# Kernel optimization log

Hardware: AMD Instinct MI355X
Metric: run time of the kernel (lower is better)

The kernel has to match this reference:

```python
import jax, jax.numpy as jnp
import numpy as np
from jax import lax

T, B, C, L = 2048, 96, 128, 128
BLANK = 0
SMOOTHING = 0.1
NEG = jnp.float32(-1e30)  # finite stand-in for -inf (safe grads, bf16-safe exponent)


def setup_inputs() -> dict:
    key = jax.random.key(0)
    k1, k2 = jax.random.split(key)
    logits = jax.random.normal(k1, (T, B, C), dtype=jnp.float32)
    log_probs = jax.nn.log_softmax(logits, axis=-1)  # [T,B,C], properly normalized
    targets = jax.random.randint(k2, (B, L), 1, C, dtype=jnp.int32)  # labels, never blank
    input_lengths = jnp.full((B,), T, dtype=jnp.int32)
    target_lengths = jnp.full((B,), L, dtype=jnp.int32)
    return {"log_probs": log_probs, "targets": targets,
            "input_lengths": input_lengths, "target_lengths": target_lengths}


def _ctc_loss(log_probs, targets, input_lengths, target_lengths):
    """Per-sample CTC negative log-likelihood. targets: [B, L] dense."""
    S = 2 * L + 1  # extended label length: blank-interleaved
    # extended labels [B, S]: blank, y1, blank, y2, ..., yL, blank
    ext = jnp.full((B, S), BLANK, dtype=jnp.int32).at[:, 1::2].set(targets)
    # gather log-probs of extended labels: [T, B, S]
    lp_ext = jnp.take_along_axis(log_probs, jnp.broadcast_to(ext[None], (T, B, S)), axis=2)
    # skip (s-2 -> s) transition allowed iff label(s) != blank and label(s) != label(s-2)
    same2 = jnp.concatenate([jnp.ones((B, 2), bool), ext[:, 2:] == ext[:, :-2]], axis=1)
    can_skip = (ext != BLANK) & (~same2)  # [B, S]

    alpha0 = jnp.full((B, S), NEG, dtype=log_probs.dtype)
    alpha0 = alpha0.at[:, 0].set(lp_ext[0, :, 0]).at[:, 1].set(lp_ext[0, :, 1])

    negcol1 = jnp.full((B, 1), NEG, dtype=log_probs.dtype)
    negcol2 = jnp.full((B, 2), NEG, dtype=log_probs.dtype)

    def step(alpha, xs):
        lp_t, t = xs  # lp_t: [B, S]
        a1 = jnp.concatenate([negcol1, alpha[:, :-1]], axis=1)
        a2 = jnp.where(can_skip, jnp.concatenate([negcol2, alpha[:, :-2]], axis=1), NEG)
        new = jnp.logaddexp(jnp.logaddexp(alpha, a1), a2) + lp_t
        active = (t < input_lengths)[:, None]  # freeze past each sample's length
        return jnp.where(active, new, alpha), None

    alphaT, _ = lax.scan(step, alpha0, (lp_ext[1:], jnp.arange(1, T)))
    bidx = jnp.arange(B)
    ll = jnp.logaddexp(alphaT[bidx, 2 * target_lengths],
                       alphaT[bidx, 2 * target_lengths - 1])  # [B]
    # zero_infinity: impossible alignments -> loss 0
    return jnp.where(ll < NEG / 2, 0.0, -ll)


def reference(log_probs, targets, input_lengths, target_lengths):
    ctc = _ctc_loss(log_probs, targets, input_lengths, target_lengths)  # [B]
    # label-smoothing KL(uniform-over-nonblank || p) pointwise term,
    # torch: kl_div(input=log_probs, target=u).sum(-1) = sum_c u*(log u - log p_c), u_blank = 0
    u = 1.0 / (C - 1)
    nonblank = (jnp.arange(C) != BLANK)  # [C]
    kl = jnp.sum(jnp.where(nonblank, u * (jnp.log(jnp.float32(u)) - log_probs), 0.0), axis=-1)  # [T,B]
    tmask = (jnp.arange(T)[:, None] < input_lengths[None, :]).astype(kl.dtype)  # [T,B]
    kl_mean = jnp.sum(kl * tmask, axis=0) / input_lengths.astype(kl.dtype)  # [B]
    loss = (1.0 - SMOOTHING) * ctc + SMOOTHING * kl_mean
    return loss.mean()
```

## Files before the change

### kernel.cpp

```cpp
#include <hip/hip_runtime.h>
#include <math.h>

#define T_DIM 2048
#define B_DIM 96
#define C_DIM 128
#define L_DIM 128
#define LOG2E 1.4426950408889634f
#define LN2 0.69314718055994531f
#define SMOOTH 0.1f
#define SENT (-(1 << 30))
#define NPH 32

#define AOFF 0
#define BOFF 24672
#define KLA  49344
#define KLB  49440
#define LOSS 49536

__device__ __forceinline__ float dpp_shr1_f(float x) {
  return __int_as_float(__builtin_amdgcn_update_dpp(
      0, __float_as_int(x), 0x138 , 0xF, 0xF, true));
}
__device__ __forceinline__ float dpp_shl1_f(float x) {
  return __int_as_float(__builtin_amdgcn_update_dpp(
      0, __float_as_int(x), 0x130 , 0xF, 0xF, true));
}

#define ALPHA_STEP(kk_) do {                                                 \
  const int k_ = (kk_);                                                      \
  const float pAv = fA[k_ & 3], pBv = fB[k_ & 3], pKv = fK[k_ & 3];          \
  {                                                                          \
    const int kn = k_ + 4;                                                   \
    const float* nr = (kn < 32) ? (pc + kn * C_DIM)                          \
                                : (pn + (kn - 32) * C_DIM);                  \
    fA[k_ & 3] = nr[tgA]; fB[k_ & 3] = nr[tgB]; fK[k_ & 3] = nr[0];          \
  }                                                                          \
  const float r3s = dpp_shr1_f(r3);                                          \
  const int   Es  = (int)dpp_shr1_f((float)E);                               \
  const int   be  = (__float_as_int(r3s) >> 23) & 0xFF;                      \
  int diff = (be - 187) + (Es - E);                                          \
  diff = (__float_as_int(r3s) != 0 && diff > 0) ? diff : 0;                  \
  r0 = ldexpf(r0, -diff); r1 = ldexpf(r1, -diff); r2 = ldexpf(r2, -diff);    \
  r3 = ldexpf(r3, -diff); r4 = ldexpf(r4, -diff);                            \
  E += diff;                                                                 \
  const float d3 = ldexpf(r3s, Es - E);                                      \
  const float n0 = (r0 + d3) * pKv;                                          \
  const float n1 = __builtin_fmaf(skA, d3, r0 + r1) * pAv;                   \
  const float n2 = (r2 + r1) * pKv;                                          \
  const float n3 = __builtin_fmaf(skB, r1, r3 + r2) * pBv;                   \
  const float n4 = (r4 + r3) * pKv;                                          \
  r0 = n0; r1 = n1; r2 = n2; r3 = n3; r4 = n4;                               \
  if ((k_ & 3) == 3) {                                                       \
    const float m = fmaxf(fmaxf(fmaxf(r0, r1), fmaxf(r2, r3)), r4);          \
    const int sh2 = (m > 0.0f)                                               \
                      ? (187 - ((__float_as_int(m) >> 23) & 0xFF)) : 0;      \
    r0 = ldexpf(r0, sh2); r1 = ldexpf(r1, sh2); r2 = ldexpf(r2, sh2);        \
    r3 = ldexpf(r3, sh2); r4 = ldexpf(r4, sh2);                              \
    E -= sh2;                                                                \
  }                                                                          \
} while (0)

#define BETA_STEP(kk_) do {                                                  \
  const int k_ = (kk_);                                                      \
  const float pAv = fA[k_ & 3], pBv = fB[k_ & 3], pKv = fK[k_ & 3];          \
  const float pNv = fN[k_ & 3];                                              \
  {                                                                          \
    const int kn = k_ + 4;                                                   \
    const float* nr = (kn < 32) ? (pc + kn * C_DIM)                          \
                                : (pn + (kn - 32) * C_DIM);                  \
    fA[k_ & 3] = nr[tgA]; fB[k_ & 3] = nr[tgB]; fK[k_ & 3] = nr[0];          \
    fN[k_ & 3] = nr[tgAn];                                                   \
  }                                                                          \
  const float r1s = dpp_shl1_f(r1);                                          \
  const int   Es  = (int)dpp_shl1_f((float)E);                               \
  const int   be  = (__float_as_int(r1s) >> 23) & 0xFF;                      \
  int diff = (be - 187) + (Es - E);                                          \
  diff = (__float_as_int(r1s) != 0 && diff > 0) ? diff : 0;                  \
  r0 = ldexpf(r0, -diff); r1 = ldexpf(r1, -diff); r2 = ldexpf(r2, -diff);    \
  r3 = ldexpf(r3, -diff); r4 = ldexpf(r4, -diff);                            \
  E += diff;                                                                 \
  const float d5 = ldexpf(r1s, Es - E);                                      \
  const float g0 = r0 * pKv, g1 = r1 * pAv, g2 = r2 * pKv;                   \
  const float g3 = r3 * pBv, g4 = r4 * pKv, g5 = d5 * pNv;                   \
  const float n0 = g0 + g1;                                                  \
  const float n1 = __builtin_fmaf(skAp, g3, g1 + g2);                        \
  const float n2 = g2 + g3;                                                  \
  const float n3 = __builtin_fmaf(skBp, g5, g3 + g4);                        \
  const float n4 = g4 + g5;                                                  \
  r0 = n0; r1 = n1; r2 = n2; r3 = n3; r4 = n4;                               \
  if ((k_ & 3) == 3) {                                                       \
    const float m = fmaxf(fmaxf(fmaxf(r0, r1), fmaxf(r2, r3)), r4);          \
    const int sh2 = (m > 0.0f)                                               \
                      ? (187 - ((__float_as_int(m) >> 23) & 0xFF)) : 0;      \
    r0 = ldexpf(r0, sh2); r1 = ldexpf(r1, sh2); r2 = ldexpf(r2, sh2);        \
    r3 = ldexpf(r3, sh2); r4 = ldexpf(r4, sh2);                              \
    E -= sh2;                                                                \
  }                                                                          \
} while (0)

__global__ __launch_bounds__(256) void ctc_fused_kernel(
    const float* __restrict__ lp, const int* __restrict__ targets,
    const int* __restrict__ in_len, const int* __restrict__ tg_len,
    float* __restrict__ ws)
{
  const int tid = threadIdx.x;
  const int bid = blockIdx.x;
  const int isBeta = (bid >= B_DIM);
  const int b = isBeta ? bid - B_DIM : bid;
  const size_t RSTR = (size_t)B_DIM * C_DIM;
  const int Tb = in_len[b];
  const float* base = lp + (size_t)b * C_DIM;

  __shared__ float rows[3][32][C_DIM];
  __shared__ float klred[3];

  float klacc = 0.f;

  if (!isBeta) {
    const int TbA = (Tb < 1024) ? Tb : 1024;
    int tgA = 0, tgB = 0;
    float skA = 0.f, skB = 0.f;
    float r0 = 0.f, r1 = 0.f, r2 = 0.f, r3 = 0.f, r4 = 0.f;
    int E = SENT;
    float fA[4], fB[4], fK[4];

    if (tid < 64) {
      const int l = tid;
      tgA = targets[b * L_DIM + 2 * l];
      tgB = targets[b * L_DIM + 2 * l + 1];
      skA = (l > 0 && tgA != targets[b * L_DIM + 2 * l - 1]) ? 1.f : 0.f;
      skB = (tgB != tgA) ? 1.f : 0.f;
      if (l == 0) {
        r0 = __builtin_amdgcn_exp2f(base[0]   * LOG2E);
        r1 = __builtin_amdgcn_exp2f(base[tgA] * LOG2E);
        E = 0;
      }
    } else {
      const int ptid = tid - 64;
      #pragma unroll
      for (int i = 0; i < 11; ++i) {
        const int task = i * 192 + ptid;
        if (task < 2048) {
          const int row = task >> 5;
          const int c4  = task & 31;
          const int t   = 1 + row;
          const float4 v = *(const float4*)(base + (size_t)t * RSTR + c4 * 4);
          float4 w;
          w.x = __builtin_amdgcn_exp2f(v.x * LOG2E);
          w.y = __builtin_amdgcn_exp2f(v.y * LOG2E);
          w.z = __builtin_amdgcn_exp2f(v.z * LOG2E);
          w.w = __builtin_amdgcn_exp2f(v.w * LOG2E);
          *(float4*)&rows[row >> 5][row & 31][c4 * 4] = w;
          if (t < Tb) {
            float s = v.x + v.y + v.z + v.w;
            if (c4 == 0) s -= v.x;
            klacc += s;
          }
        }
      }
      if (ptid < 32 && 0 < Tb) {
        const float4 v = *(const float4*)(base + ptid * 4);
        float s = v.x + v.y + v.z + v.w;
        if (ptid == 0) s -= v.x;
        klacc += s;
      }
    }
    __syncthreads();

    if (tid < 64) {
      #pragma unroll
      for (int j = 0; j < 4; ++j) {
        fA[j] = rows[0][j][tgA]; fB[j] = rows[0][j][tgB]; fK[j] = rows[0][j][0];
      }
    }
    float* pc = &rows[0][0][0];
    float* pn = &rows[1][0][0];
    float* pf = &rows[2][0][0];

    for (int p = 0; p < NPH; ++p) {
      if (tid < 64) {
        if (32 * p + 33 <= TbA) {
          #pragma unroll
          for (int k = 0; k < 32; ++k) { ALPHA_STEP(k); }
        } else {
          #pragma unroll
          for (int k = 0; k < 32; ++k) {
            const int t = 1 + 32 * p + k;
            if (t < TbA) { ALPHA_STEP(k); }
          }
        }
      } else {
        const int ptid = tid - 64;
        const int t0 = 65 + 32 * p;
        if (t0 <= 1023) {
          #pragma unroll
          for (int i = 0; i < 6; ++i) {
            const int task = i * 192 + ptid;
            if (task < 1024) {
              const int row = task >> 5;
              const int c4  = task & 31;
              const int t   = t0 + row;
              if (t <= 1023) {
                const float4 v = *(const float4*)(base + (size_t)t * RSTR + c4 * 4);
                float4 w;
                w.x = __builtin_amdgcn_exp2f(v.x * LOG2E);
                w.y = __builtin_amdgcn_exp2f(v.y * LOG2E);
                w.z = __builtin_amdgcn_exp2f(v.z * LOG2E);
                w.w = __builtin_amdgcn_exp2f(v.w * LOG2E);
                *(float4*)&pf[row * C_DIM + c4 * 4] = w;
                if (t < Tb) {
                  float s = v.x + v.y + v.z + v.w;
                  if (c4 == 0) s -= v.x;
                  klacc += s;
                }
              }
            }
          }
        }
      }
      __syncthreads();
      float* tmp = pc; pc = pn; pn = pf; pf = tmp;
    }

    if (tid < 64) {
      const int l = tid;
      const float Ef = (float)E;
      float* dst = ws + AOFF + b * 257;
      dst[4 * l + 0] = __builtin_amdgcn_logf(r0) + Ef;
      dst[4 * l + 1] = __builtin_amdgcn_logf(r1) + Ef;
      dst[4 * l + 2] = __builtin_amdgcn_logf(r2) + Ef;
      dst[4 * l + 3] = __builtin_amdgcn_logf(r3) + Ef;
      if (l == 63) dst[256] = __builtin_amdgcn_logf(r4) + Ef;
    } else {
      float tot = klacc;
      tot += __shfl_xor(tot, 1, 64);  tot += __shfl_xor(tot, 2, 64);
      tot += __shfl_xor(tot, 4, 64);  tot += __shfl_xor(tot, 8, 64);
      tot += __shfl_xor(tot, 16, 64); tot += __shfl_xor(tot, 32, 64);
      if ((tid & 63) == 0) klred[(tid >> 6) - 1] = tot;
    }
    __syncthreads();
    if (tid == 0) ws[KLA + b] = klred[0] + klred[1] + klred[2];

  } else {
    int tgA = 0, tgB = 0, tgAn = 0;
    float skAp = 0.f, skBp = 0.f;
    float r0 = 0.f, r1 = 0.f, r2 = 0.f, r3 = 0.f, r4 = 0.f;
    int E = SENT;
    float fA[4], fB[4], fK[4], fN[4];

    if (tid < 64) {
      const int l = tid;
      tgA = targets[b * L_DIM + 2 * l];
      tgB = targets[b * L_DIM + 2 * l + 1];
      const int nidx = (l < 63) ? (2 * l + 2) : (2 * l);
      tgAn = targets[b * L_DIM + nidx];
      skAp = (tgB != tgA) ? 1.f : 0.f;
      skBp = (l < 63 && tgAn != tgB) ? 1.f : 0.f;
      const int Lt = tg_len[b];
      const int s0 = 4 * l;
      r0 = (s0 == 2 * Lt || s0 == 2 * Lt - 1) ? 1.f : 0.f;
      r1 = (s0 + 1 == 2 * Lt || s0 + 1 == 2 * Lt - 1) ? 1.f : 0.f;
      r2 = (s0 + 2 == 2 * Lt || s0 + 2 == 2 * Lt - 1) ? 1.f : 0.f;
      r3 = (s0 + 3 == 2 * Lt || s0 + 3 == 2 * Lt - 1) ? 1.f : 0.f;
      r4 = (s0 + 4 == 2 * Lt || s0 + 4 == 2 * Lt - 1) ? 1.f : 0.f;
      E = (r0 + r1 + r2 + r3 + r4 > 0.f) ? 0 : SENT;
    } else {
      const int ptid = tid - 64;
      #pragma unroll
      for (int i = 0; i < 11; ++i) {
        const int task = i * 192 + ptid;
        if (task < 2048) {
          const int row = task >> 5;
          const int c4  = task & 31;
          const int t   = 2047 - row;
          const float4 v = *(const float4*)(base + (size_t)t * RSTR + c4 * 4);
          float4 w;
          w.x = __builtin_amdgcn_exp2f(v.x * LOG2E);
          w.y = __builtin_amdgcn_exp2f(v.y * LOG2E);
          w.z = __builtin_amdgcn_exp2f(v.z * LOG2E);
          w.w = __builtin_amdgcn_exp2f(v.w * LOG2E);
          *(float4*)&rows[row >> 5][row & 31][c4 * 4] = w;
          if (t < Tb) {
            float s = v.x + v.y + v.z + v.w;
            if (c4 == 0) s -= v.x;
            klacc += s;
          }
        }
      }
    }
    __syncthreads();

    if (tid < 64) {
      #pragma unroll
      for (int j = 0; j < 4; ++j) {
        fA[j] = rows[0][j][tgA]; fB[j] = rows[0][j][tgB];
        fK[j] = rows[0][j][0];   fN[j] = rows[0][j][tgAn];
      }
    }
    float* pc = &rows[0][0][0];
    float* pn = &rows[1][0][0];
    float* pf = &rows[2][0][0];

    for (int p = 0; p < NPH; ++p) {
      if (tid < 64) {
        const int rmax = 2047 - 32 * p;
        const int rmin = rmax - 31;
        if (rmax < Tb) {
          #pragma unroll
          for (int k = 0; k < 32; ++k) { BETA_STEP(k); }
        } else if (rmin < Tb) {
          #pragma unroll
          for (int k = 0; k < 32; ++k) {
            const int r = 2047 - 32 * p - k;
            if (r < Tb) { BETA_STEP(k); }
          }
        }
      } else {
        const int ptid = tid - 64;
        const int t0 = 1983 - 32 * p;
        if (t0 >= 1024) {
          #pragma unroll
          for (int i = 0; i < 6; ++i) {
            const int task = i * 192 + ptid;
            if (task < 1024) {
              const int row = task >> 5;
              const int c4  = task & 31;
              const int t   = t0 - row;
              if (t >= 1024) {
                const float4 v = *(const float4*)(base + (size_t)t * RSTR + c4 * 4);
                float4 w;
                w.x = __builtin_amdgcn_exp2f(v.x * LOG2E);
                w.y = __builtin_amdgcn_exp2f(v.y * LOG2E);
                w.z = __builtin_amdgcn_exp2f(v.z * LOG2E);
                w.w = __builtin_amdgcn_exp2f(v.w * LOG2E);
                *(float4*)&pf[row * C_DIM + c4 * 4] = w;
                if (t < Tb) {
                  float s = v.x + v.y + v.z + v.w;
                  if (c4 == 0) s -= v.x;
                  klacc += s;
                }
              }
            }
          }
        }
      }
      __syncthreads();
      float* tmp = pc; pc = pn; pn = pf; pf = tmp;
    }

    if (tid < 64) {
      const int l = tid;
      const float Ef = (float)E;
      float* dst = ws + BOFF + b * 257;
      dst[4 * l + 0] = __builtin_amdgcn_logf(r0) + Ef;
      dst[4 * l + 1] = __builtin_amdgcn_logf(r1) + Ef;
      dst[4 * l + 2] = __builtin_amdgcn_logf(r2) + Ef;
      dst[4 * l + 3] = __builtin_amdgcn_logf(r3) + Ef;
      if (l == 63) dst[256] = __builtin_amdgcn_logf(r4) + Ef;
    } else {
      float tot = klacc;
      tot += __shfl_xor(tot, 1, 64);  tot += __shfl_xor(tot, 2, 64);
      tot += __shfl_xor(tot, 4, 64);  tot += __shfl_xor(tot, 8, 64);
      tot += __shfl_xor(tot, 16, 64); tot += __shfl_xor(tot, 32, 64);
      if ((tid & 63) == 0) klred[(tid >> 6) - 1] = tot;
    }
    __syncthreads();
    if (tid == 0) ws[KLB + b] = klred[0] + klred[1] + klred[2];
  }
}

__global__ __launch_bounds__(64) void ctc_combine_kernel(
    const float* __restrict__ ws_in, const int* __restrict__ in_len,
    float* __restrict__ ws_out)
{
  const int b = blockIdx.x;
  const int l = threadIdx.x;
  const float* a  = ws_in + AOFF + b * 257;
  const float* bb = ws_in + BOFF + b * 257;
  float x0 = a[4 * l + 0] + bb[4 * l + 0];
  float x1 = a[4 * l + 1] + bb[4 * l + 1];
  float x2 = a[4 * l + 2] + bb[4 * l + 2];
  float x3 = a[4 * l + 3] + bb[4 * l + 3];
  float x4 = (l == 63) ? (a[256] + bb[256]) : -3.0e38f;
  float m = fmaxf(fmaxf(fmaxf(x0, x1), fmaxf(x2, x3)), x4);
  m = fmaxf(m, __shfl_xor(m, 1, 64));  m = fmaxf(m, __shfl_xor(m, 2, 64));
  m = fmaxf(m, __shfl_xor(m, 4, 64));  m = fmaxf(m, __shfl_xor(m, 8, 64));
  m = fmaxf(m, __shfl_xor(m, 16, 64)); m = fmaxf(m, __shfl_xor(m, 32, 64));
  const float ms = fmaxf(m, -1.0e37f);
  float s = __builtin_amdgcn_exp2f(x0 - ms) + __builtin_amdgcn_exp2f(x1 - ms)
          + __builtin_amdgcn_exp2f(x2 - ms) + __builtin_amdgcn_exp2f(x3 - ms)
          + __builtin_amdgcn_exp2f(x4 - ms);
  s += __shfl_xor(s, 1, 64);  s += __shfl_xor(s, 2, 64);
  s += __shfl_xor(s, 4, 64);  s += __shfl_xor(s, 8, 64);
  s += __shfl_xor(s, 16, 64); s += __shfl_xor(s, 32, 64);
  if (l == 0) {
    float ctc = 0.f;
    if (s > 0.f && m > -1.0e30f) {
      ctc = -((ms + __builtin_amdgcn_logf(s)) * LN2);
    }
    const int Tb = in_len[b];
    const float u    = 1.0f / (C_DIM - 1);
    const float logu = -4.8441870864585910f;
    const float kls  = ws_in[KLA + b] + ws_in[KLB + b];
    const float klmean = logu - u * kls / (float)Tb;
    ws_out[LOSS + b] = (1.0f - SMOOTH) * ctc + SMOOTH * klmean;
  }
}

__global__ __launch_bounds__(128) void ctc_mean_kernel(
    const float* __restrict__ ws, float* __restrict__ out)
{
  __shared__ float red[128];
  const int tid = threadIdx.x;
  red[tid] = (tid < B_DIM) ? ws[LOSS + tid] : 0.f;
  __syncthreads();
  for (int off = 64; off > 0; off >>= 1) {
    if (tid < off) red[tid] += red[tid + off];
    __syncthreads();
  }
  if (tid == 0) out[0] = red[0] / (float)B_DIM;
}

extern "C" void kernel_launch(void* const* d_in, const int* in_sizes, int n_in,
                              void* d_out, int out_size, void* d_ws, size_t ws_size,
                              hipStream_t stream) {
  const float* lp      = (const float*)d_in[0];
  const int* targets   = (const int*)d_in[1];
  const int* in_len    = (const int*)d_in[2];
  const int* tg_len    = (const int*)d_in[3];
  float* ws  = (float*)d_ws;
  float* out = (float*)d_out;

  hipLaunchKernelGGL(ctc_fused_kernel, dim3(2 * B_DIM), dim3(256), 0, stream,
                     lp, targets, in_len, tg_len, ws);
  hipLaunchKernelGGL(ctc_combine_kernel, dim3(B_DIM), dim3(64), 0, stream,
                     ws, in_len, ws);
  hipLaunchKernelGGL(ctc_mean_kernel, dim3(1), dim3(128), 0, stream,
                     ws, out);
}
```

Baseline: 88.68 us.

## Merge alpha and beta blocks into one 512-thread block per sample

Instead of launching separate 256-thread blocks for the forward (alpha) and backward (beta) halves, each sample now gets one 512-thread block. The two 256-thread groups run the alpha and beta recursions with separate dynamic shared-memory ring buffers. This halves the block count to 96, so on a GPU with many CUs fewer CUs are used, but both halves share a block. Each __syncthreads now couples the two independent halves, which can add stall time, and the larger 96KB shared footprint limits residency.

```diff
diff --git a/kernel.cpp b/kernel.cpp
--- a/kernel.cpp
+++ b/kernel.cpp
@@ -98,25 +98,26 @@
   }                                                                          \
 } while (0)
 
-__global__ __launch_bounds__(256) void ctc_fused_kernel(
+__global__ __launch_bounds__(512, 2) void ctc_fused_kernel(
     const float* __restrict__ lp, const int* __restrict__ targets,
     const int* __restrict__ in_len, const int* __restrict__ tg_len,
     float* __restrict__ ws)
 {
-  const int tid = threadIdx.x;
-  const int bid = blockIdx.x;
-  const int isBeta = (bid >= B_DIM);
-  const int b = isBeta ? bid - B_DIM : bid;
+  extern __shared__ float dyn[];
+  const int tid  = threadIdx.x;
+  const int grp  = tid >> 8;
+  const int gtid = tid & 255;
+  const int b = blockIdx.x;
   const size_t RSTR = (size_t)B_DIM * C_DIM;
   const int Tb = in_len[b];
   const float* base = lp + (size_t)b * C_DIM;
 
-  __shared__ float rows[3][32][C_DIM];
-  __shared__ float klred[3];
+  float* ring = dyn + grp * (3 * 32 * C_DIM);
+  __shared__ float klred[2][3];
 
   float klacc = 0.f;
 
-  if (!isBeta) {
+  if (grp == 0) {
     const int TbA = (Tb < 1024) ? Tb : 1024;
     int tgA = 0, tgB = 0;
     float skA = 0.f, skB = 0.f;
@@ -124,8 +125,8 @@
     int E = SENT;
     float fA[4], fB[4], fK[4];
 
-    if (tid < 64) {
-      const int l = tid;
+    if (gtid < 64) {
+      const int l = gtid;
       tgA = targets[b * L_DIM + 2 * l];
       tgB = targets[b * L_DIM + 2 * l + 1];
       skA = (l > 0 && tgA != targets[b * L_DIM + 2 * l - 1]) ? 1.f : 0.f;
@@ -136,7 +137,7 @@
         E = 0;
       }
     } else {
-      const int ptid = tid - 64;
+      const int ptid = gtid - 64;
       #pragma unroll
       for (int i = 0; i < 11; ++i) {
         const int task = i * 192 + ptid;
@@ -150,7 +151,7 @@
           w.y = __builtin_amdgcn_exp2f(v.y * LOG2E);
           w.z = __builtin_amdgcn_exp2f(v.z * LOG2E);
           w.w = __builtin_amdgcn_exp2f(v.w * LOG2E);
-          *(float4*)&rows[row >> 5][row & 31][c4 * 4] = w;
+          *(float4*)&ring[(row >> 5) * 32 * C_DIM + (row & 31) * C_DIM + c4 * 4] = w;
           if (t < Tb) {
             float s = v.x + v.y + v.z + v.w;
             if (c4 == 0) s -= v.x;
@@ -167,18 +168,19 @@
     }
     __syncthreads();
 
-    if (tid < 64) {
+    if (gtid < 64) {
       #pragma unroll
       for (int j = 0; j < 4; ++j) {
-        fA[j] = rows[0][j][tgA]; fB[j] = rows[0][j][tgB]; fK[j] = rows[0][j][0];
-      }
-    }
-    float* pc = &rows[0][0][0];
-    float* pn = &rows[1][0][0];
-    float* pf = &rows[2][0][0];
+        fA[j] = ring[j * C_DIM + tgA]; fB[j] = ring[j * C_DIM + tgB];
+        fK[j] = ring[j * C_DIM];
+      }
+    }
+    float* pc = ring;
+    float* pn = ring + 32 * C_DIM;
+    float* pf = ring + 64 * C_DIM;
 
     for (int p = 0; p < NPH; ++p) {
-      if (tid < 64) {
+      if (gtid < 64) {
         if (32 * p + 33 <= TbA) {
           #pragma unroll
           for (int k = 0; k < 32; ++k) { ALPHA_STEP(k); }
@@ -190,7 +192,7 @@
           }
         }
       } else {
-        const int ptid = tid - 64;
+        const int ptid = gtid - 64;
         const int t0 = 65 + 32 * p;
         if (t0 <= 1023) {
           #pragma unroll
@@ -222,8 +224,8 @@
       float* tmp = pc; pc = pn; pn = pf; pf = tmp;
     }
 
-    if (tid < 64) {
-      const int l = tid;
+    if (gtid < 64) {
+      const int l = gtid;
       const float Ef = (float)E;
       float* dst = ws + AOFF + b * 257;
       dst[4 * l + 0] = __builtin_amdgcn_logf(r0) + Ef;
@@ -236,10 +238,10 @@
       tot += __shfl_xor(tot, 1, 64);  tot += __shfl_xor(tot, 2, 64);
       tot += __shfl_xor(tot, 4, 64);  tot += __shfl_xor(tot, 8, 64);
       tot += __shfl_xor(tot, 16, 64); tot += __shfl_xor(tot, 32, 64);
-      if ((tid & 63) == 0) klred[(tid >> 6) - 1] = tot;
+      if ((gtid & 63) == 0) klred[0][(gtid >> 6) - 1] = tot;
     }
     __syncthreads();
-    if (tid == 0) ws[KLA + b] = klred[0] + klred[1] + klred[2];
+    if (gtid == 0) ws[KLA + b] = klred[0][0] + klred[0][1] + klred[0][2];
 
   } else {
     int tgA = 0, tgB = 0, tgAn = 0;
@@ -248,8 +250,8 @@
     int E = SENT;
     float fA[4], fB[4], fK[4], fN[4];
 
-    if (tid < 64) {
-      const int l = tid;
+    if (gtid < 64) {
+      const int l = gtid;
       tgA = targets[b * L_DIM + 2 * l];
       tgB = targets[b * L_DIM + 2 * l + 1];
       const int nidx = (l < 63) ? (2 * l + 2) : (2 * l);
@@ -265,7 +267,7 @@
       r4 = (s0 + 4 == 2 * Lt || s0 + 4 == 2 * Lt - 1) ? 1.f : 0.f;
       E = (r0 + r1 + r2 + r3 + r4 > 0.f) ? 0 : SENT;
     } else {
-      const int ptid = tid - 64;
+      const int ptid = gtid - 64;
       #pragma unroll
       for (int i = 0; i < 11; ++i) {
         const int task = i * 192 + ptid;
@@ -279,7 +281,7 @@
           w.y = __builtin_amdgcn_exp2f(v.y * LOG2E);
           w.z = __builtin_amdgcn_exp2f(v.z * LOG2E);
           w.w = __builtin_amdgcn_exp2f(v.w * LOG2E);
-          *(float4*)&rows[row >> 5][row & 31][c4 * 4] = w;
+          *(float4*)&ring[(row >> 5) * 32 * C_DIM + (row & 31) * C_DIM + c4 * 4] = w;
           if (t < Tb) {
             float s = v.x + v.y + v.z + v.w;
             if (c4 == 0) s -= v.x;
@@ -290,19 +292,19 @@
     }
     __syncthreads();
 
-    if (tid < 64) {
+    if (gtid < 64) {
       #pragma unroll
       for (int j = 0; j < 4; ++j) {
-        fA[j] = rows[0][j][tgA]; fB[j] = rows[0][j][tgB];
-        fK[j] = rows[0][j][0];   fN[j] = rows[0][j][tgAn];
-      }
-    }
-    float* pc = &rows[0][0][0];
-    float* pn = &rows[1][0][0];
-    float* pf = &rows[2][0][0];
+        fA[j] = ring[j * C_DIM + tgA]; fB[j] = ring[j * C_DIM + tgB];
+        fK[j] = ring[j * C_DIM];       fN[j] = ring[j * C_DIM + tgAn];
+      }
+    }
+    float* pc = ring;
+    float* pn = ring + 32 * C_DIM;
+    float* pf = ring + 64 * C_DIM;
 
     for (int p = 0; p < NPH; ++p) {
-      if (tid < 64) {
+      if (gtid < 64) {
         const int rmax = 2047 - 32 * p;
         const int rmin = rmax - 31;
         if (rmax < Tb) {
@@ -316,7 +318,7 @@
           }
         }
       } else {
-        const int ptid = tid - 64;
+        const int ptid = gtid - 64;
         const int t0 = 1983 - 32 * p;
         if (t0 >= 1024) {
           #pragma unroll
@@ -348,8 +350,8 @@
       float* tmp = pc; pc = pn; pn = pf; pf = tmp;
     }
 
-    if (tid < 64) {
-      const int l = tid;
+    if (gtid < 64) {
+      const int l = gtid;
       const float Ef = (float)E;
       float* dst = ws + BOFF + b * 257;
       dst[4 * l + 0] = __builtin_amdgcn_logf(r0) + Ef;
@@ -362,10 +364,10 @@
       tot += __shfl_xor(tot, 1, 64);  tot += __shfl_xor(tot, 2, 64);
       tot += __shfl_xor(tot, 4, 64);  tot += __shfl_xor(tot, 8, 64);
       tot += __shfl_xor(tot, 16, 64); tot += __shfl_xor(tot, 32, 64);
-      if ((tid & 63) == 0) klred[(tid >> 6) - 1] = tot;
+      if ((gtid & 63) == 0) klred[1][(gtid >> 6) - 1] = tot;
     }
     __syncthreads();
-    if (tid == 0) ws[KLB + b] = klred[0] + klred[1] + klred[2];
+    if (gtid == 0) ws[KLB + b] = klred[1][0] + klred[1][1] + klred[1][2];
   }
 }
 
@@ -431,7 +433,16 @@
   float* ws  = (float*)d_ws;
   float* out = (float*)d_out;
 
-  hipLaunchKernelGGL(ctc_fused_kernel, dim3(2 * B_DIM), dim3(256), 0, stream,
+  const size_t dynBytes = 2u * 3u * 32u * C_DIM * sizeof(float);
+  static bool attrSet = false;
+  if (!attrSet) {
+    (void)hipFuncSetAttribute((const void*)ctc_fused_kernel,
+                              hipFuncAttributeMaxDynamicSharedMemorySize,
+                              (int)dynBytes);
+    attrSet = true;
+  }
+
+  hipLaunchKernelGGL(ctc_fused_kernel, dim3(B_DIM), dim3(512), dynBytes, stream,
                      lp, targets, in_len, tg_len, ws);
   hipLaunchKernelGGL(ctc_combine_kernel, dim3(B_DIM), dim3(64), 0, stream,
                      ws, in_len, ws);
```

New measurement: 139.9 us. 57.7% more time.

## Amortize per-step exponent alignment into a once-per-4-steps neighbor scale exchange

Applied to the files above, without the earlier changes.

Each alpha and beta step used to exchange the neighbor lane's exponent over DPP and rescale all five registers with ldexp before using the shifted value. Now the exponent alignment runs only every four steps, alongside the existing renormalization, and yields a multiplicative scale factor. The per-step neighbor term becomes a single multiply. This shortens the serial dependency chain of the recurrence, at the cost of a lower renormalization target exponent and more reliance on float headroom between syncs.

```diff
diff --git a/kernel.cpp b/kernel.cpp
--- a/kernel.cpp
+++ b/kernel.cpp
@@ -9,6 +9,7 @@
 #define LN2 0.69314718055994531f
 #define SMOOTH 0.1f
 #define SENT (-(1 << 30))
+#define SENTF (-1073741824.0f)
 #define NPH 32
 
 #define AOFF 0
@@ -25,6 +26,50 @@
   return __int_as_float(__builtin_amdgcn_update_dpp(
       0, __float_as_int(x), 0x130 , 0xF, 0xF, true));
 }
+
+#define AEXCH() do {                                                         \
+  const float m = fmaxf(fmaxf(fmaxf(r0, r1), fmaxf(r2, r3)), r4);            \
+  const int sh2 = (m > 0.0f) ? (177 - ((__float_as_int(m) >> 23) & 0xFF)) : 0;\
+  r0 = ldexpf(r0, sh2); r1 = ldexpf(r1, sh2); r2 = ldexpf(r2, sh2);          \
+  r3 = ldexpf(r3, sh2); r4 = ldexpf(r4, sh2);                                \
+  E -= sh2;                                                                  \
+  float Esf = dpp_shr1_f((float)E);                                          \
+  Esf = (tid == 0) ? SENTF : Esf;                                            \
+  const int Es = (int)Esf;                                                   \
+  const bool live = (Es != SENT);                                            \
+  if (E == SENT && live) E = Es;                                             \
+  int sh = (Es - E) - 60; sh = (sh > 0) ? sh : 0; sh = (sh > 252) ? 252 : sh;\
+  r0 = ldexpf(r0, -sh); r1 = ldexpf(r1, -sh); r2 = ldexpf(r2, -sh);          \
+  r3 = ldexpf(r3, -sh); r4 = ldexpf(r4, -sh);                                \
+  E += sh;                                                                   \
+  const int diff = Es - E;                                                   \
+  int dc = (diff < -126) ? -126 : diff;                                      \
+  float sc = __int_as_float((127 + dc) << 23);                               \
+  sc = (diff < -126) ? 0.0f : sc;                                            \
+  scale = live ? sc : 0.0f;                                                  \
+} while (0)
+
+#define BEXCH() do {                                                         \
+  const float m = fmaxf(fmaxf(fmaxf(r0, r1), fmaxf(r2, r3)), r4);            \
+  const int sh2 = (m > 0.0f) ? (177 - ((__float_as_int(m) >> 23) & 0xFF)) : 0;\
+  r0 = ldexpf(r0, sh2); r1 = ldexpf(r1, sh2); r2 = ldexpf(r2, sh2);          \
+  r3 = ldexpf(r3, sh2); r4 = ldexpf(r4, sh2);                                \
+  E -= sh2;                                                                  \
+  float Esf = dpp_shl1_f((float)E);                                          \
+  Esf = (tid == 63) ? SENTF : Esf;                                           \
+  const int Es = (int)Esf;                                                   \
+  const bool live = (Es != SENT);                                            \
+  if (E == SENT && live) E = Es;                                             \
+  int sh = (Es - E) - 60; sh = (sh > 0) ? sh : 0; sh = (sh > 252) ? 252 : sh;\
+  r0 = ldexpf(r0, -sh); r1 = ldexpf(r1, -sh); r2 = ldexpf(r2, -sh);          \
+  r3 = ldexpf(r3, -sh); r4 = ldexpf(r4, -sh);                                \
+  E += sh;                                                                   \
+  const int diff = Es - E;                                                   \
+  int dc = (diff < -126) ? -126 : diff;                                      \
+  float sc = __int_as_float((127 + dc) << 23);                               \
+  sc = (diff < -126) ? 0.0f : sc;                                            \
+  scale = live ? sc : 0.0f;                                                  \
+} while (0)
 
 #define ALPHA_STEP(kk_) do {                                                 \
   const int k_ = (kk_);                                                      \
@@ -36,28 +81,14 @@
     fA[k_ & 3] = nr[tgA]; fB[k_ & 3] = nr[tgB]; fK[k_ & 3] = nr[0];          \
   }                                                                          \
   const float r3s = dpp_shr1_f(r3);                                          \
-  const int   Es  = (int)dpp_shr1_f((float)E);                               \
-  const int   be  = (__float_as_int(r3s) >> 23) & 0xFF;                      \
-  int diff = (be - 187) + (Es - E);                                          \
-  diff = (__float_as_int(r3s) != 0 && diff > 0) ? diff : 0;                  \
-  r0 = ldexpf(r0, -diff); r1 = ldexpf(r1, -diff); r2 = ldexpf(r2, -diff);    \
-  r3 = ldexpf(r3, -diff); r4 = ldexpf(r4, -diff);                            \
-  E += diff;                                                                 \
-  const float d3 = ldexpf(r3s, Es - E);                                      \
+  const float d3  = r3s * scale;                                             \
   const float n0 = (r0 + d3) * pKv;                                          \
   const float n1 = __builtin_fmaf(skA, d3, r0 + r1) * pAv;                   \
   const float n2 = (r2 + r1) * pKv;                                          \
   const float n3 = __builtin_fmaf(skB, r1, r3 + r2) * pBv;                   \
   const float n4 = (r4 + r3) * pKv;                                          \
   r0 = n0; r1 = n1; r2 = n2; r3 = n3; r4 = n4;                               \
-  if ((k_ & 3) == 3) {                                                       \
-    const float m = fmaxf(fmaxf(fmaxf(r0, r1), fmaxf(r2, r3)), r4);          \
-    const int sh2 = (m > 0.0f)                                               \
-                      ? (187 - ((__float_as_int(m) >> 23) & 0xFF)) : 0;      \
-    r0 = ldexpf(r0, sh2); r1 = ldexpf(r1, sh2); r2 = ldexpf(r2, sh2);        \
-    r3 = ldexpf(r3, sh2); r4 = ldexpf(r4, sh2);                              \
-    E -= sh2;                                                                \
-  }                                                                          \
+  if ((k_ & 3) == 3) { AEXCH(); }                                            \
 } while (0)
 
 #define BETA_STEP(kk_) do {                                                  \
@@ -72,14 +103,7 @@
     fN[k_ & 3] = nr[tgAn];                                                   \
   }                                                                          \
   const float r1s = dpp_shl1_f(r1);                                          \
-  const int   Es  = (int)dpp_shl1_f((float)E);                               \
-  const int   be  = (__float_as_int(r1s) >> 23) & 0xFF;                      \
-  int diff = (be - 187) + (Es - E);                                          \
-  diff = (__float_as_int(r1s) != 0 && diff > 0) ? diff : 0;                  \
-  r0 = ldexpf(r0, -diff); r1 = ldexpf(r1, -diff); r2 = ldexpf(r2, -diff);    \
-  r3 = ldexpf(r3, -diff); r4 = ldexpf(r4, -diff);                            \
-  E += diff;                                                                 \
-  const float d5 = ldexpf(r1s, Es - E);                                      \
+  const float d5  = r1s * scale;                                             \
   const float g0 = r0 * pKv, g1 = r1 * pAv, g2 = r2 * pKv;                   \
   const float g3 = r3 * pBv, g4 = r4 * pKv, g5 = d5 * pNv;                   \
   const float n0 = g0 + g1;                                                  \
@@ -88,14 +112,7 @@
   const float n3 = __builtin_fmaf(skBp, g5, g3 + g4);                        \
   const float n4 = g4 + g5;                                                  \
   r0 = n0; r1 = n1; r2 = n2; r3 = n3; r4 = n4;                               \
-  if ((k_ & 3) == 3) {                                                       \
-    const float m = fmaxf(fmaxf(fmaxf(r0, r1), fmaxf(r2, r3)), r4);          \
-    const int sh2 = (m > 0.0f)                                               \
-                      ? (187 - ((__float_as_int(m) >> 23) & 0xFF)) : 0;      \
-    r0 = ldexpf(r0, sh2); r1 = ldexpf(r1, sh2); r2 = ldexpf(r2, sh2);        \
-    r3 = ldexpf(r3, sh2); r4 = ldexpf(r4, sh2);                              \
-    E -= sh2;                                                                \
-  }                                                                          \
+  if ((k_ & 3) == 3) { BEXCH(); }                                            \
 } while (0)
 
 __global__ __launch_bounds__(256) void ctc_fused_kernel(
@@ -122,6 +139,7 @@
     float skA = 0.f, skB = 0.f;
     float r0 = 0.f, r1 = 0.f, r2 = 0.f, r3 = 0.f, r4 = 0.f;
     int E = SENT;
+    float scale = 0.f;
     float fA[4], fB[4], fK[4];
 
     if (tid < 64) {
@@ -172,6 +190,7 @@
       for (int j = 0; j < 4; ++j) {
         fA[j] = rows[0][j][tgA]; fB[j] = rows[0][j][tgB]; fK[j] = rows[0][j][0];
       }
+      AEXCH();
     }
     float* pc = &rows[0][0][0];
     float* pn = &rows[1][0][0];
@@ -246,6 +265,7 @@
     float skAp = 0.f, skBp = 0.f;
     float r0 = 0.f, r1 = 0.f, r2 = 0.f, r3 = 0.f, r4 = 0.f;
     int E = SENT;
+    float scale = 0.f;
     float fA[4], fB[4], fK[4], fN[4];
 
     if (tid < 64) {
@@ -296,6 +316,7 @@
         fA[j] = rows[0][j][tgA]; fB[j] = rows[0][j][tgB];
         fK[j] = rows[0][j][0];   fN[j] = rows[0][j][tgAn];
       }
+      BEXCH();
     }
     float* pc = &rows[0][0][0];
     float* pn = &rows[1][0][0];
```

Result: faster. 84.43 us (-4.8%).
